# Kernel tuning notes

Measured on AMD Instinct MI355X. Metric: run time of the kernel, lower is better.

The kernel has to match this reference:

```python
import jax, jax.numpy as jnp
import numpy as np

N, T, D, P, Q = 256, 4096, 64, 4, 4
COEF_SCALE = 0.15  # keeps ARMA stationary over long T


def setup_inputs() -> dict:
    key = jax.random.key(0)
    k_eps, k_phi, k_theta, k_mu = jax.random.split(key, 4)
    eps = jax.random.normal(k_eps, (N, T, D), dtype=jnp.float32)
    phi = COEF_SCALE * jax.random.normal(k_phi, (D, P), dtype=jnp.float32)
    theta = COEF_SCALE * jax.random.normal(k_theta, (D, Q), dtype=jnp.float32)
    mu = jax.random.normal(k_mu, (D,), dtype=jnp.float32)
    x0 = jnp.zeros((N, D), dtype=jnp.float32)
    return {"eps": eps, "phi": phi, "theta": theta, "mu": mu, "x0": x0}


def reference(eps, phi, theta, mu, x0):
    # eps: (N,T,d); phi: (d,p); theta: (d,q); mu: (d,); x0: (N,d)
    n, t, d = eps.shape
    p = phi.shape[1]
    q = theta.shape[1]
    # x history: most-recent-first, [x0, 0, ..., 0] (matches torch padding of x_hist)
    xh0 = jnp.concatenate([x0[:, :, None], jnp.zeros((n, d, p - 1), eps.dtype)], axis=-1)
    eh0 = jnp.zeros((n, d, q), eps.dtype)  # eps history starts as zeros

    def step(carry, e_t):
        xh, eh = carry  # (n,d,p), (n,d,q)
        ar = jnp.einsum('ndp,dp->nd', xh, phi)
        ma = jnp.einsum('ndq,dq->nd', eh, theta)
        x_t = mu[None, :] + ar + e_t + ma  # (n,d)
        xh = jnp.concatenate([x_t[:, :, None], xh[:, :, :-1]], axis=-1)
        eh = jnp.concatenate([e_t[:, :, None], eh[:, :, :-1]], axis=-1)
        return (xh, eh), x_t

    _, xs = jax.lax.scan(step, (xh0, eh0), jnp.swapaxes(eps, 0, 1))  # xs: (T,N,d)
    return jnp.swapaxes(xs, 0, 1)  # (N,T,d)
```

## Files before the change

kernel.cpp:

```cpp
#include <hip/hip_runtime.h>
#include <stdint.h>


constexpr int N = 256;
constexpr int T = 4096;
constexpr int D = 64;
constexpr int P = 4;
constexpr int Q = 4;

constexpr int K = 8;
constexpr int L = 512;
constexpr int B = 256;
constexpr int U = 32;
constexpr int NDMA = (U * D * sizeof(float)) / 1024;

__global__ __launch_bounds__(64, 2)
void arma_lds_kernel(const float* __restrict__ eps,
                     const float* __restrict__ phi,
                     const float* __restrict__ theta,
                     const float* __restrict__ mu,
                     const float* __restrict__ x0,
                     float* __restrict__ out) {
    const int lane = threadIdx.x;
    const int k = blockIdx.x % K;
    const int n = blockIdx.x / K;

    const float ph0 = phi[lane * P + 0];
    const float ph1 = phi[lane * P + 1];
    const float ph2 = phi[lane * P + 2];
    const float ph3 = phi[lane * P + 3];
    const float th0 = theta[lane * Q + 0];
    const float th1 = theta[lane * Q + 1];
    const float th2 = theta[lane * Q + 2];
    const float th3 = theta[lane * Q + 3];
    const float m   = mu[lane];

    const int t0   = k * L;
    const int ts   = (k == 0) ? 0 : t0 - B;
    const int tend = t0 + L;
    const int nit  = (tend - ts) / U;

    const float* gbase = eps + (size_t)n * T * D;
    float*       obase = out + (size_t)n * T * D;

    const int lt  = lane >> 4;
    const int ld4 = (lane & 15) * 4;

    __shared__ float lbuf[2][U * D];

    float x1, x2, x3, x4, e1, e2, e3, e4;
    x1 = x2 = x3 = x4 = 0.f;
    e1 = e2 = e3 = e4 = 0.f;
    if (k == 0) {
        x1 = x0[n * D + lane];
    } else {
        e1 = gbase[(size_t)(ts - 1) * D + lane];
        e2 = gbase[(size_t)(ts - 2) * D + lane];
        e3 = gbase[(size_t)(ts - 3) * D + lane];
        e4 = gbase[(size_t)(ts - 4) * D + lane];
    }

    auto issue = [&](int b, int t) {
#pragma unroll
        for (int i = 0; i < NDMA; ++i) {
            const float* src = gbase + (size_t)(t + i * 4 + lt) * D + ld4;
            __builtin_amdgcn_global_load_lds(
                (const __attribute__((address_space(1))) void*)src,
                (__attribute__((address_space(3))) void*)&lbuf[b][i * 256],
                16, 0, 0);
        }
    };

    auto compute = [&](int b, int t, bool emit) {
#pragma unroll
        for (int u = 0; u < U; ++u) {
            const float e = lbuf[b][u * D + lane];
            float acc = m + e;
            acc = fmaf(th0, e1, acc);
            acc = fmaf(th1, e2, acc);
            acc = fmaf(th2, e3, acc);
            acc = fmaf(th3, e4, acc);
            acc = fmaf(ph3, x4, acc);
            acc = fmaf(ph2, x3, acc);
            acc = fmaf(ph1, x2, acc);
            const float x = fmaf(ph0, x1, acc);
            x4 = x3; x3 = x2; x2 = x1; x1 = x;
            e4 = e3; e3 = e2; e2 = e1; e1 = e;
            if (emit) obase[(size_t)(t + u) * D + lane] = x;
        }
    };

    issue(0, ts);
    {
        const int tn = (ts + U < tend) ? ts + U : ts;
        issue(1, tn);
    }
    asm volatile("s_waitcnt vmcnt(8)" ::: "memory");
    __builtin_amdgcn_sched_barrier(0);
    bool prev_emit = (ts >= t0);
    compute(0, ts, prev_emit);

    for (int it = 1; it < nit; ++it) {
        const int t  = ts + it * U;
        const int tn = (t + U < tend) ? t + U : ts;
        issue((it + 1) & 1, tn);
        if (prev_emit) {
            asm volatile("s_waitcnt vmcnt(40)" ::: "memory");
        } else {
            asm volatile("s_waitcnt vmcnt(8)" ::: "memory");
        }
        __builtin_amdgcn_sched_barrier(0);
        const bool em = (t >= t0);
        compute(it & 1, t, em);
        prev_emit = em;
    }
}

extern "C" void kernel_launch(void* const* d_in, const int* in_sizes, int n_in,
                              void* d_out, int out_size, void* d_ws, size_t ws_size,
                              hipStream_t stream) {
    const float* eps   = (const float*)d_in[0];
    const float* phi   = (const float*)d_in[1];
    const float* theta = (const float*)d_in[2];
    const float* mu    = (const float*)d_in[3];
    const float* x0    = (const float*)d_in[4];
    float* out = (float*)d_out;

    arma_lds_kernel<<<dim3(N * K), dim3(64), 0, stream>>>(eps, phi, theta, mu, x0, out);
}
```

Before: 125.8 us.

## Deepen LDS prefetch pipeline to four smaller buffers and use nontemporal stores

Replaces the two 32-step LDS buffers with four 16-step buffers, keeping three chunks of eps in flight ahead of the compute. The vmcnt wait thresholds are recomputed to account for the store instructions that are outstanding once output emission begins. Output stores become nontemporal to reduce cache pollution. The change trades larger total prefetch depth for more frequent wait points, and it depends on hand-counted vmcnt values being correct.

```diff
diff --git a/kernel.cpp b/kernel.cpp
--- a/kernel.cpp
+++ b/kernel.cpp
@@ -11,16 +11,17 @@
 constexpr int K = 8;
 constexpr int L = 512;
 constexpr int B = 256;
-constexpr int U = 32;
+constexpr int U = 16;
+constexpr int NB = 4;
 constexpr int NDMA = (U * D * sizeof(float)) / 1024;
 
 __global__ __launch_bounds__(64, 2)
-void arma_lds_kernel(const float* __restrict__ eps,
-                     const float* __restrict__ phi,
-                     const float* __restrict__ theta,
-                     const float* __restrict__ mu,
-                     const float* __restrict__ x0,
-                     float* __restrict__ out) {
+void arma_deep_kernel(const float* __restrict__ eps,
+                      const float* __restrict__ phi,
+                      const float* __restrict__ theta,
+                      const float* __restrict__ mu,
+                      const float* __restrict__ x0,
+                      float* __restrict__ out) {
     const int lane = threadIdx.x;
     const int k = blockIdx.x % K;
     const int n = blockIdx.x / K;
@@ -39,6 +40,7 @@
     const int ts   = (k == 0) ? 0 : t0 - B;
     const int tend = t0 + L;
     const int nit  = (tend - ts) / U;
+    const int SB   = (t0 - ts) / U;
 
     const float* gbase = eps + (size_t)n * T * D;
     float*       obase = out + (size_t)n * T * D;
@@ -46,7 +48,7 @@
     const int lt  = lane >> 4;
     const int ld4 = (lane & 15) * 4;
 
-    __shared__ float lbuf[2][U * D];
+    __shared__ float lbuf[NB][U * D];
 
     float x1, x2, x3, x4, e1, e2, e3, e4;
     x1 = x2 = x3 = x4 = 0.f;
@@ -86,33 +88,33 @@
             const float x = fmaf(ph0, x1, acc);
             x4 = x3; x3 = x2; x2 = x1; x1 = x;
             e4 = e3; e3 = e2; e2 = e1; e1 = e;
-            if (emit) obase[(size_t)(t + u) * D + lane] = x;
+            if (emit) __builtin_nontemporal_store(x, &obase[(size_t)(t + u) * D + lane]);
         }
     };
 
     issue(0, ts);
-    {
-        const int tn = (ts + U < tend) ? ts + U : ts;
-        issue(1, tn);
-    }
-    asm volatile("s_waitcnt vmcnt(8)" ::: "memory");
-    __builtin_amdgcn_sched_barrier(0);
-    bool prev_emit = (ts >= t0);
-    compute(0, ts, prev_emit);
+    issue(1, ts + U);
+    issue(2, ts + 2 * U);
 
-    for (int it = 1; it < nit; ++it) {
-        const int t  = ts + it * U;
-        const int tn = (t + U < tend) ? t + U : ts;
-        issue((it + 1) & 1, tn);
-        if (prev_emit) {
-            asm volatile("s_waitcnt vmcnt(40)" ::: "memory");
+    for (int j = 0; j < nit; ++j) {
+        const int t = ts + j * U;
+        int tpre = t + 3 * U;
+        if (tpre > tend - U) tpre = tend - U;
+        issue((j + 3) & (NB - 1), tpre);
+
+        const int d = j - SB;
+        if (d <= 0) {
+            asm volatile("s_waitcnt vmcnt(12)" ::: "memory");
+        } else if (d == 1) {
+            asm volatile("s_waitcnt vmcnt(28)" ::: "memory");
+        } else if (d == 2) {
+            asm volatile("s_waitcnt vmcnt(44)" ::: "memory");
         } else {
-            asm volatile("s_waitcnt vmcnt(8)" ::: "memory");
+            asm volatile("s_waitcnt vmcnt(60)" ::: "memory");
         }
         __builtin_amdgcn_sched_barrier(0);
-        const bool em = (t >= t0);
-        compute(it & 1, t, em);
-        prev_emit = em;
+
+        compute(j & (NB - 1), t, j >= SB);
     }
 }
 
@@ -126,5 +128,5 @@
     const float* x0    = (const float*)d_in[4];
     float* out = (float*)d_out;
 
-    arma_lds_kernel<<<dim3(N * K), dim3(64), 0, stream>>>(eps, phi, theta, mu, x0, out);
+    arma_deep_kernel<<<dim3(N * K), dim3(64), 0, stream>>>(eps, phi, theta, mu, x0, out);
 }
```

Result: faster. 113.1 us (-10.0%).
